# Performance work log

Hardware: AMD Instinct MI355X
Metric: run time of the kernel (lower is better)

## Reference

```python
import jax, jax.numpy as jnp
import numpy as np


def _dwconv_silu(feat, w, b):
    # feat: (B, L, C); depthwise 1D conv, kernel 7, pad 3, then SiLU (PointLiteConv)
    x = jnp.swapaxes(feat, 1, 2)  # (B, C, L)
    y = jax.lax.conv_general_dilated(x, w, (1,), [(3, 3)],
                                     feature_group_count=x.shape[1],
                                     dimension_numbers=('NCH', 'OIH', 'NCH'))
    y = y + b[None, :, None]
    return jnp.swapaxes(jax.nn.silu(y), 1, 2)


def _issm_scan(x, h0, dt, A, Bm, Cm, Dp):
    # x: (B,L,H,P)  h0: (B,H,P,N)  dt: (B,L,H,N)  A: (H,1)  Bm,Cm: (B,L,1,N)  Dp: (H,)
    dA = jnp.exp(dt * A)                      # (B,L,H,N) discrete decay
    u = dt * Bm                               # (B,L,H,N) input coeff (ngroups=1 broadcast)
    Cb = jnp.broadcast_to(Cm, dt.shape)       # (B,L,H,N)

    def step(h, inp):
        dA_t, u_t, x_t, c_t = inp             # (B,H,N),(B,H,N),(B,H,P),(B,H,N)
        h = dA_t[:, :, None, :] * h + x_t[..., None] * u_t[:, :, None, :]
        return h, jnp.einsum('bhpn,bhn->bhp', h, c_t)

    xs = tuple(jnp.moveaxis(a, 1, 0) for a in (dA, u, x, Cb))
    hF, ys = jax.lax.scan(step, h0, xs)
    y = jnp.moveaxis(ys, 0, 1) + Dp[None, None, :, None] * x
    return y, hF


def setup_inputs() -> dict:
    key = jax.random.key(0)
    ks = jax.random.split(key, 20)
    B, L, K = 2, 2048, 64
    d_model, d_state, d_dist, H, G, d_inner = 512, 64, 4, 8, 1, 1024
    c_conv = d_inner + 2 * G  # 1026
    s = 0.02
    dt0 = jnp.exp(jax.random.uniform(ks[12], (H,)) * (np.log(0.1) - np.log(1e-4)) + np.log(1e-4))
    dt0 = jnp.clip(dt0, 1e-4, None)
    return {
        'in_key': jax.random.normal(ks[0], (B, L, d_model), jnp.float32),
        'in_query': jax.random.normal(ks[1], (B, K, d_model), jnp.float32),
        'dist': jax.random.uniform(ks[2], (B, L, K, d_dist), jnp.float32),
        'key_xyz': jax.random.normal(ks[3], (B, L, 3), jnp.float32),
        'key_proj_w': jax.random.normal(ks[4], (2 * d_inner + 2 * G + H, d_model), jnp.float32) * s,
        'key_conv_w': jax.random.normal(ks[5], (c_conv, 1, 7), jnp.float32) * s,
        'key_conv_b': jnp.zeros((c_conv,), jnp.float32),
        'key_conv_back_w': jax.random.normal(ks[6], (c_conv, 1, 7), jnp.float32) * s,
        'key_conv_back_b': jnp.zeros((c_conv,), jnp.float32),
        'query_proj_w': jax.random.normal(ks[7], (d_inner, d_model), jnp.float32) * s,
        'bc_proj_w': jax.random.normal(ks[8], (2 * G, d_dist), jnp.float32) * s,
        'dt_proj_w': jax.random.normal(ks[9], (H, d_dist), jnp.float32) * s,
        'dt_bias': dt0 + jnp.log(-jnp.expm1(-dt0)),
        'A_log': jnp.log(jax.random.uniform(ks[10], (H,), jnp.float32, 1.0, 16.0)),
        'D_param': jnp.ones((H,), jnp.float32),
        'out_key_w': jax.random.normal(ks[11], (d_model, d_inner), jnp.float32) * s,
        'out_query_w': jax.random.normal(ks[13], (d_model, d_inner), jnp.float32) * s,
        'key_norm_w': jnp.ones((d_inner,), jnp.float32),
        'q_ln_w': jnp.ones((d_inner,), jnp.float32),
        'q_ln_b': jnp.zeros((d_inner,), jnp.float32),
    }


def reference(in_key, in_query, dist, key_xyz, key_proj_w, key_conv_w, key_conv_b,
              key_conv_back_w, key_conv_back_b, query_proj_w, bc_proj_w, dt_proj_w,
              dt_bias, A_log, D_param, out_key_w, out_query_w, key_norm_w, q_ln_w, q_ln_b):
    B, L, _ = in_key.shape
    K = in_query.shape[1]
    d_inner = query_proj_w.shape[0]
    H = dt_bias.shape[0]
    G = bc_proj_w.shape[0] // 2
    P = d_inner // H

    zxbcdt = in_key @ key_proj_w.T                       # (B,L,2*di+2G+H)
    z = zxbcdt[..., :d_inner]
    xbc = zxbcdt[..., d_inner:2 * d_inner + 2 * G]
    dt_head = zxbcdt[..., 2 * d_inner + 2 * G:]          # (B,L,H)

    xbc_f = _dwconv_silu(xbc, key_conv_w, key_conv_b)
    x = xbc_f[..., :d_inner]
    b_bias = xbc_f[..., d_inner:d_inner + G]
    c_bias = xbc_f[..., d_inner + G:]
    xbc_b = _dwconv_silu(xbc, key_conv_back_w, key_conv_back_b)
    x_bk = xbc_b[..., :d_inner]
    b_bias_b = xbc_b[..., d_inner:d_inner + G]
    c_bias_b = xbc_b[..., d_inner + G:]

    # initial state: 'b l (h hd) -> b h hd l'  -> (B,H,P,K)
    h0 = (in_query @ query_proj_w.T).reshape(B, K, H, P).transpose(0, 2, 3, 1)
    A = -jnp.exp(A_log)[:, None]                         # (H,1), repeated over d_state

    bc = dist @ bc_proj_w.T                              # (B,L,K,2G)
    b_base = jnp.swapaxes(bc[..., :G], -1, -2)           # (B,L,G,K)
    c_base = jnp.swapaxes(bc[..., G:], -1, -2)
    Bm = b_base + b_bias[..., None]
    Cm = c_base + c_bias[..., None]
    Bmb = b_base + b_bias_b[..., None]
    Cmb = c_base + c_bias_b[..., None]

    dt = jax.nn.softplus(jnp.swapaxes(dist @ dt_proj_w.T, -1, -2)
                         + dt_head[..., None] + dt_bias[None, None, :, None])  # (B,L,H,K)

    xh = x.reshape(B, L, H, P)
    y_f, h_f = _issm_scan(xh, h0, dt, A, Bm, Cm, D_param)
    xb = jnp.flip(x_bk.reshape(B, L, H, P), 1)
    y_b, h_b = _issm_scan(xb, h0, jnp.flip(dt, 1), A, jnp.flip(Bmb, 1), jnp.flip(Cmb, 1), D_param)
    y = (y_f + jnp.flip(y_b, 1)) * 0.5                   # (B,L,H,P)
    h_last = (h_f + h_b) * 0.5                           # (B,H,P,K)

    key_feat = y.reshape(B, L, d_inner)
    xg = key_feat * jax.nn.silu(z)                       # gated RMSNorm (gate before norm)
    key_n = xg * jax.lax.rsqrt(jnp.mean(xg * xg, -1, keepdims=True) + 1e-5) * key_norm_w
    out_key = key_n @ out_key_w.T

    q = h_last.transpose(0, 3, 1, 2).reshape(B, K, d_inner)  # 'b h p l -> b l (h p)'
    mu = jnp.mean(q, -1, keepdims=True)
    var = jnp.mean((q - mu) ** 2, -1, keepdims=True)
    qn = (q - mu) * jax.lax.rsqrt(var + 1e-5) * q_ln_w + q_ln_b
    out_query = qn @ out_query_w.T
    return out_key, out_query
```

## Files before the change

kernel.cpp:

```cpp
#include <hip/hip_runtime.h>
#include <hip/hip_bf16.h>
#include <cstdint>

constexpr int B_ = 2, L_ = 2048, K_ = 64, H_ = 8, P_ = 128, DI = 1024;
constexpr int NPROJ = 2058;
constexpr int NC = L_ / 64;
constexpr int XBCS = 1040;

typedef unsigned short u16;
typedef short bf16x8 __attribute__((ext_vector_type(8)));
typedef float f32x4 __attribute__((ext_vector_type(4)));

__constant__ int c_sz[20] = {2097152,65536,1048576,12288,1053696,7182,1026,7182,1026,
                             524288,8,32,8,8,8,524288,524288,1024,1024,1024};
__constant__ int c_of[20] = {16,2097168,2162704,3211280,3223568,4277264,4284446,4285472,
                             4292654,4293680,4817968,4817976,4818008,4818016,4818024,
                             4818032,5342320,5866608,5867632,5868656};
constexpr int OF_INKEY = 16, OF_INQ = 2097168, OF_DIST = 2162704, OF_KPW = 3223568;
constexpr int OF_CONVW = 4277264, OF_CONVB = 4284446, OF_CONVBW = 4285472, OF_CONVBB = 4292654;
constexpr int OF_QPW = 4293680, OF_BCW = 4817968, OF_DTW = 4817976, OF_DTBIAS = 4818008;
constexpr int OF_ALOG = 4818016, OF_D = 4818024, OF_OKW = 4818032, OF_OQW = 5342320;
constexpr int OF_KNW = 5866608, OF_QLW = 5867632, OF_QLB = 5868656;
constexpr int SEG_A = 2097152, SEG_W = 2176*512, SEG_O = 524288;
constexpr int SEG_Q = 65536, SEG_P = 524288, SEG_D = 1048576;
constexpr int NSMALL = 18552;
constexpr int NSTAGE = SEG_O + SEG_O + 4096 + NSMALL + (SEG_A + SEG_Q + SEG_D + SEG_W + SEG_P);

constexpr int WZ     = 5869696;
constexpr int WXBC   = 10064000;
constexpr int WDTH   = 14266496;
constexpr int WXF    = 14299264;
constexpr int WXBK   = 18493568;
constexpr int WBBF   = 22687872;
constexpr int WCBF   = 22691968;
constexpr int WBBB   = 22696064;
constexpr int WCBB   = 22700160;
constexpr int WDT    = 22704256;
constexpr int WBBASE = 24801408;
constexpr int WCBASE = 25063552;
constexpr int WH0I   = 25325696;
constexpr int WE     = 25456768;
constexpr int WDH    = 25522304;
constexpr int WYF    = 42299520;
constexpr int WYB    = 46493824;
constexpr int WHFIN  = 50688128;
constexpr int WSROW  = 50950272;
constexpr int WEND   = 50954368;

#define DEV __device__ __forceinline__
DEV float4 ld4(const float* p) { return *(const float4*)p; }
DEV void st4(float* p, float4 v) { *(float4*)p = v; }
DEV float silu_(float x) { return x / (1.f + __expf(-x)); }
DEV u16 f2b(float f) {
    unsigned x = __float_as_uint(f);
    return (u16)((x + 0x7fffu + ((x >> 16) & 1u)) >> 16);
}
DEV float b2f(u16 v) { return __uint_as_float(((unsigned)v) << 16); }
DEV float4 b2f4(const u16* p) {
    uint2 u = *(const uint2*)p;
    float4 r;
    r.x = __uint_as_float(u.x << 16);
    r.y = __uint_as_float(u.x & 0xffff0000u);
    r.z = __uint_as_float(u.y << 16);
    r.w = __uint_as_float(u.y & 0xffff0000u);
    return r;
}
DEV float4 b2f4u(uint2 u) {
    float4 r;
    r.x = __uint_as_float(u.x << 16);
    r.y = __uint_as_float(u.x & 0xffff0000u);
    r.z = __uint_as_float(u.y << 16);
    r.w = __uint_as_float(u.y & 0xffff0000u);
    return r;
}
DEV uint2 pku2(float4 v) {
    uint2 u;
    u.x = (unsigned)f2b(v.x) | ((unsigned)f2b(v.y) << 16);
    u.y = (unsigned)f2b(v.z) | ((unsigned)f2b(v.w) << 16);
    return u;
}
DEV void st4b(u16* p, float4 v) { *(uint2*)p = pku2(v); }

#define GLL16(gp, lp) __builtin_amdgcn_global_load_lds( \
    (const __attribute__((address_space(1))) unsigned int*)(gp), \
    (__attribute__((address_space(3))) unsigned int*)(lp), 16, 0, 0)

struct SrcPtrs { const void* p[20]; };
DEV bool bfmode(const SrcPtrs& sp) { return ((const u16*)sp.p[17])[0] == 0x3F80u; }

__global__ void k_sentinel(float* out) { out[threadIdx.x] = 1e9f; }

__global__ __launch_bounds__(256) void k_stage(SrcPtrs sp, float* ws) {
    int g = blockIdx.x * 256 + threadIdx.x;
    bool bf = bfmode(sp);
    if (g < SEG_O) {
        int col = g & 1023;
        float wv = bf ? b2f(((const u16*)sp.p[15])[g]) : ((const float*)sp.p[15])[g];
        float kn = bf ? b2f(((const u16*)sp.p[17])[col]) : ((const float*)sp.p[17])[col];
        ((u16*)(ws + OF_OKW))[g] = f2b(wv * kn);
        return;
    }
    g -= SEG_O;
    if (g < SEG_O) {
        ((u16*)(ws + OF_OQW))[g] = bf ? ((const u16*)sp.p[16])[g]
                                      : f2b(((const float*)sp.p[16])[g]);
        return;
    }
    g -= SEG_O;
    if (g < 4096) { ws[WSROW + g] = 0.f; return; }
    g -= 4096;
    if (g < NSMALL) {
        const int sidx[12] = {5,6,7,8,10,11,12,13,14,17,18,19};
        int rem = g;
        #pragma unroll
        for (int ii = 0; ii < 12; ++ii) {
            int s = sidx[ii];
            int sz = c_sz[s];
            if (rem < sz) {
                float v = bf ? b2f(((const u16*)sp.p[s])[rem])
                             : ((const float*)sp.p[s])[rem];
                ws[c_of[s] + rem] = v;
                return;
            }
            rem -= sz;
        }
        return;
    }
    g -= NSMALL;
    if (bf) return;
    if (g < SEG_A) { ((u16*)(ws + OF_INKEY))[g] = f2b(((const float*)sp.p[0])[g]); return; }
    g -= SEG_A;
    if (g < SEG_Q) { ((u16*)(ws + OF_INQ))[g] = f2b(((const float*)sp.p[1])[g]); return; }
    g -= SEG_Q;
    if (g < SEG_D) { ws[OF_DIST + g] = ((const float*)sp.p[2])[g]; return; }
    g -= SEG_D;
    if (g < SEG_W) {
        int row = g >> 9, col = g & 511;
        ((u16*)(ws + OF_KPW))[g] = (row < NPROJ) ? f2b(((const float*)sp.p[4])[row*512 + col]) : (u16)0;
        return;
    }
    g -= SEG_W;
    if (g < SEG_P) { ((u16*)(ws + OF_QPW))[g] = f2b(((const float*)sp.p[9])[g]); return; }
}

__global__ __launch_bounds__(256) void k_gemm_proj(SrcPtrs sp, float* ws) {
    __shared__ u16 As[128*32], Bs[128*32];
    bool bf = bfmode(sp);
    int tid = threadIdx.x, w = tid >> 6, l = tid & 63;
    int wm = w & 1, wn = w >> 1;
    int lr = l & 15, lq = l >> 4;
    int srow = tid >> 2, scol = (tid & 3) * 8;
    if (blockIdx.y == 32) {
        if (blockIdx.x >= 8) return;
        const u16* Ab = bf ? (const u16*)sp.p[1] : (const u16*)(ws + OF_INQ);
        const u16* Wb = bf ? (const u16*)sp.p[9] : (const u16*)(ws + OF_QPW);
        int n0 = blockIdx.x * 128;
        f32x4 acc[4][4];
        #pragma unroll
        for (int i = 0; i < 4; ++i)
            #pragma unroll
            for (int j = 0; j < 4; ++j) acc[i][j] = {0.f,0.f,0.f,0.f};
        for (int kt = 0; kt < 512; kt += 32) {
            __syncthreads();
            GLL16(Ab + (size_t)(srow)*512      + kt + scol, As + (w*512));
            GLL16(Ab + (size_t)(64 + srow)*512 + kt + scol, As + (2048 + w*512));
            GLL16(Wb + (size_t)(n0 + srow)*512      + kt + scol, Bs + (w*512));
            GLL16(Wb + (size_t)(n0 + 64 + srow)*512 + kt + scol, Bs + (2048 + w*512));
            __syncthreads();
            bf16x8 af[4], bfr[4];
            #pragma unroll
            for (int mi = 0; mi < 4; ++mi) af[mi]  = *(const bf16x8*)&As[(wm*64 + mi*16 + lr)*32 + lq*8];
            #pragma unroll
            for (int ni = 0; ni < 4; ++ni) bfr[ni] = *(const bf16x8*)&Bs[(wn*64 + ni*16 + lr)*32 + lq*8];
            #pragma unroll
            for (int mi = 0; mi < 4; ++mi)
                #pragma unroll
                for (int ni = 0; ni < 4; ++ni)
                    acc[mi][ni] = __builtin_amdgcn_mfma_f32_16x16x32_bf16(af[mi], bfr[ni], acc[mi][ni], 0, 0, 0);
        }
        #pragma unroll
        for (int mi = 0; mi < 4; ++mi)
            #pragma unroll
            for (int ni = 0; ni < 4; ++ni)
                #pragma unroll
                for (int r = 0; r < 4; ++r) {
                    int m = wm*64 + mi*16 + lq*4 + r;
                    int n = n0 + wn*64 + ni*16 + lr;
                    int b = m >> 6, kq = m & 63, h = n >> 7, p = n & 127;
                    ws[WH0I + ((b*8 + h)*64 + kq)*128 + p] = acc[mi][ni][r];
                }
        return;
    }
    const u16* Ab = bf ? (const u16*)sp.p[0] : (const u16*)(ws + OF_INKEY);
    const u16* Wb = bf ? (const u16*)sp.p[4] : (const u16*)(ws + OF_KPW);
    int n0 = blockIdx.x * 128, m0 = blockIdx.y * 128;
    int wr0 = n0 + srow;      if (wr0 > NPROJ-1) wr0 = NPROJ-1;
    int wr1 = n0 + 64 + srow; if (wr1 > NPROJ-1) wr1 = NPROJ-1;
    f32x4 acc[4][4];
    #pragma unroll
    for (int i = 0; i < 4; ++i)
        #pragma unroll
        for (int j = 0; j < 4; ++j) acc[i][j] = {0.f,0.f,0.f,0.f};
    for (int kt = 0; kt < 512; kt += 32) {
        __syncthreads();
        GLL16(Ab + (size_t)(m0 + srow)*512      + kt + scol, As + (w*512));
        GLL16(Ab + (size_t)(m0 + 64 + srow)*512 + kt + scol, As + (2048 + w*512));
        GLL16(Wb + (size_t)wr0*512 + kt + scol, Bs + (w*512));
        GLL16(Wb + (size_t)wr1*512 + kt + scol, Bs + (2048 + w*512));
        __syncthreads();
        bf16x8 af[4], bfr[4];
        #pragma unroll
        for (int mi = 0; mi < 4; ++mi) af[mi]  = *(const bf16x8*)&As[(wm*64 + mi*16 + lr)*32 + lq*8];
        #pragma unroll
        for (int ni = 0; ni < 4; ++ni) bfr[ni] = *(const bf16x8*)&Bs[(wn*64 + ni*16 + lr)*32 + lq*8];
        #pragma unroll
        for (int mi = 0; mi < 4; ++mi)
            #pragma unroll
            for (int ni = 0; ni < 4; ++ni)
                acc[mi][ni] = __builtin_amdgcn_mfma_f32_16x16x32_bf16(af[mi], bfr[ni], acc[mi][ni], 0, 0, 0);
    }
    u16* xbc = (u16*)(ws + WXBC);
    u16* zb  = (u16*)(ws + WZ);
    #pragma unroll
    for (int mi = 0; mi < 4; ++mi)
        #pragma unroll
        for (int ni = 0; ni < 4; ++ni)
            #pragma unroll
            for (int r = 0; r < 4; ++r) {
                int m = m0 + wm*64 + mi*16 + lq*4 + r;
                int n = n0 + wn*64 + ni*16 + lr;
                if (n >= NPROJ) continue;
                float v = acc[mi][ni][r];
                if (n < 1024)       zb[m*1024 + n] = f2b(v);
                else if (n < 2050)  xbc[m*XBCS + (n-1024)] = f2b(v);
                else                ws[WDTH + m*8 + (n-2050)] = v;
            }
}

__global__ __launch_bounds__(256) void k_mid(SrcPtrs sp, float* ws) {
    int bx = blockIdx.x, tid = threadIdx.x;
    if (bx < 1280) {
        int cb = bx >> 8, tile = bx & 255;
        int bl0 = tile * 16;
        int l0 = bl0 & (L_ - 1);
        int base = bl0 - l0;
        int cch = cb * 256 + tid;
        if (cb == 4) { if (tid >= 2) return; cch = 1024 + tid; }
        const u16* xbc = (const u16*)(ws + WXBC);
        const float* wfp = ws + OF_CONVW + cch*7;
        const float* wbp = ws + OF_CONVBW + cch*7;
        float wf[7], wb[7];
        #pragma unroll
        for (int j = 0; j < 7; ++j) { wf[j] = wfp[j]; wb[j] = wbp[j]; }
        float bfv = ws[OF_CONVB + cch], bbv = ws[OF_CONVBB + cch];
        float win[22];
        #pragma unroll
        for (int j = 0; j < 22; ++j) {
            int l2 = l0 - 3 + j;
            win[j] = (l2 >= 0 && l2 < L_) ? b2f(xbc[(base + l2)*XBCS + cch]) : 0.f;
        }
        u16* XF = (u16*)(ws + WXF);
        u16* XB = (u16*)(ws + WXBK);
        #pragma unroll
        for (int i = 0; i < 16; ++i) {
            float af = bfv, ab = bbv;
            #pragma unroll
            for (int j = 0; j < 7; ++j) { af += win[i+j]*wf[j]; ab += win[i+j]*wb[j]; }
            af = silu_(af); ab = silu_(ab);
            if (cb < 4) {
                XF[(bl0 + i)*1024 + cch] = f2b(af);
                XB[(bl0 + i)*1024 + cch] = f2b(ab);
            } else if (cch == 1024) {
                ws[WBBF + bl0 + i] = af; ws[WBBB + bl0 + i] = ab;
            } else {
                ws[WCBF + bl0 + i] = af; ws[WCBB + bl0 + i] = ab;
            }
        }
        return;
    }
    {
        bool bf = bfmode(sp);
        int g = (bx - 1280) * 256 + tid;
        int k = g & 63, bl = g >> 6;
        float4 d4;
        if (bf) d4 = b2f4((const u16*)sp.p[2] + (size_t)g*4);
        else    d4 = ld4(&ws[OF_DIST + g*4]);
        const float* bcw = ws + OF_BCW;
        ws[WBBASE + g] = d4.x*bcw[0] + d4.y*bcw[1] + d4.z*bcw[2] + d4.w*bcw[3];
        ws[WCBASE + g] = d4.x*bcw[4] + d4.y*bcw[5] + d4.z*bcw[6] + d4.w*bcw[7];
        const float* dtw = ws + OF_DTW;
        const float* dtb = ws + OF_DTBIAS;
        const float* dth = ws + WDTH + bl*8;
        #pragma unroll
        for (int h = 0; h < 8; ++h) {
            float t = d4.x*dtw[h*4] + d4.y*dtw[h*4+1] + d4.z*dtw[h*4+2] + d4.w*dtw[h*4+3]
                    + dth[h] + dtb[h];
            float sp2 = (t > 20.f) ? t : log1pf(__expf(t));
            ws[WDT + (bl*8 + h)*64 + k] = sp2;
        }
    }
}

__global__ __launch_bounds__(256, 3) void k_scanA(float* ws) {
    __shared__ float scs[4096];
    __shared__ u16 sUeD[64*72];
    __shared__ u16 sCe[64*72];
    __shared__ u16 sM[64*72];
    __shared__ u16 sUeO[32*72];
    __shared__ float sG[128];
    u16* sXt = (u16*)scs;
    int bx = blockIdx.x;
    int c = bx & 31, dir = (bx >> 5) & 1, h = (bx >> 6) & 7, b = bx >> 9;
    int tid = threadIdx.x, w = tid >> 6, l = tid & 63;
    int lr = l & 15, tq = l >> 4;
    float Ah = -__expf(ws[OF_ALOG + h]);
    float Dv = ws[OF_D + h];
    const float* dt = ws + WDT;
    const float* bbase = ws + WBBASE; const float* cbase = ws + WCBASE;
    const float* bbias = ws + (dir ? WBBB : WBBF);
    const float* cbias = ws + (dir ? WCBB : WCBF);
    for (int q = tid; q < 1024; q += 256) {
        int t = q >> 4, k4 = (q & 15) << 2;
        int gt = dir ? (L_ - 1 - (c*64 + t)) : (c*64 + t);
        int bl = b*L_ + gt;
        float4 dv = ld4(&dt[(bl*8 + h)*64 + k4]);
        float4 bb4 = ld4(&bbase[bl*64 + k4]);
        float4 cb4 = ld4(&cbase[bl*64 + k4]);
        float bbv = bbias[bl], cbv = cbias[bl];
        st4(&scs[t*64 + k4], make_float4(dv.x*Ah, dv.y*Ah, dv.z*Ah, dv.w*Ah));
        st4b(&sUeD[t*72 + k4], make_float4(dv.x*(bb4.x+bbv), dv.y*(bb4.y+bbv),
                                           dv.z*(bb4.z+bbv), dv.w*(bb4.w+bbv)));
        st4b(&sCe[t*72 + k4], make_float4(cb4.x+cbv, cb4.y+cbv, cb4.z+cbv, cb4.w+cbv));
    }
    __syncthreads();
    {
        float* tmp = (float*)sUeO;
        int kk = tid & 63, seg = tid >> 6;
        float run = 0.f;
        for (int t = seg*16; t < seg*16 + 16; ++t) { run += scs[t*64 + kk]; scs[t*64 + kk] = run; }
        tmp[seg*64 + kk] = run;
        __syncthreads();
        float off = 0.f;
        for (int s2 = 0; s2 < seg; ++s2) off += tmp[s2*64 + kk];
        if (seg == 3) ws[WE + (((b*8 + h)*2 + dir)*32 + c)*64 + kk] = __expf(off + run);
        __syncthreads();
        if (seg > 0)
            for (int t = seg*16; t < seg*16 + 16; ++t) scs[t*64 + kk] += off;
    }
    __syncthreads();
    for (int q = tid; q < 2048; q += 256) {
        int s = q >> 6, k = q & 63;
        sUeO[s*72 + k] = f2b(b2f(sUeD[s*72 + k]) * __expf(scs[2048 + k] - scs[s*64 + k]));
    }
    if (tid < 128) {
        int j = tid >> 6, k = tid & 63;
        sG[tid] = __expf(scs[63*64 + k] - scs[j*2048 + k]);
    }
    {
        uint4 z4 = make_uint4(0,0,0,0);
        for (int q = tid; q < 576; q += 256) ((uint4*)sM)[q] = z4;
    }
    __syncthreads();
    for (int q = tid; q < 4096; q += 256) {
        int t = q >> 6, k = q & 63;
        int t0 = (t >> 5) << 5;
        sCe[t*72 + k] = f2b(b2f(sCe[t*72 + k]) * __expf(scs[t*64 + k] - scs[t0*64 + k]));
    }
    for (int q = tid; q < 4096; q += 256) {
        int s = q >> 6, k = q & 63;
        int t0 = (s >> 5) << 5;
        sUeD[s*72 + k] = f2b(b2f(sUeD[s*72 + k]) * __expf(scs[t0*64 + k] - scs[s*64 + k]));
    }
    __syncthreads();
    {
        constexpr unsigned TTP = 1047188u;
        constexpr unsigned SSP = 936208u;
        for (int i = w; i < 10; i += 4) {
            int ttile = (TTP >> (2*i)) & 3, stile = (SSP >> (2*i)) & 3;
            const u16* Bb = (ttile >= 2 && stile < 2) ? sUeO : sUeD;
            f32x4 acc = {0.f, 0.f, 0.f, 0.f};
            #pragma unroll
            for (int kh = 0; kh < 2; ++kh) {
                bf16x8 a  = *(const bf16x8*)&sCe[(ttile*16 + lr)*72 + kh*32 + tq*8];
                bf16x8 bb = *(const bf16x8*)&Bb [(stile*16 + lr)*72 + kh*32 + tq*8];
                acc = __builtin_amdgcn_mfma_f32_16x16x32_bf16(a, bb, acc, 0, 0, 0);
            }
            #pragma unroll
            for (int r = 0; r < 4; ++r) {
                int row = ttile*16 + tq*4 + r, col = stile*16 + lr;
                sM[row*72 + col] = f2b(row >= col ? acc[r] : 0.f);
            }
        }
    }
    __syncthreads();
    for (int q = tid; q < 4096; q += 256) {
        int k = q >> 6, s = q & 63;
        sCe[k*72 + s] = f2b(b2f(sUeD[s*72 + k]) * sG[((s >> 5) << 6) + k]);
    }
    __syncthreads();
    bf16x8 aM[2], aU[2];
    #pragma unroll
    for (int kh = 0; kh < 2; ++kh) {
        aM[kh] = *(const bf16x8*)&sM [(w*16 + lr)*72 + kh*32 + tq*8];
        aU[kh] = *(const bf16x8*)&sCe[(w*16 + lr)*72 + kh*32 + tq*8];
    }
    __syncthreads();
    u16* sYst = sM;
    u16* sDst = sCe;
    u16* yloc16 = (u16*)(ws + (dir ? WYB : WYF));
    const u16* Xsrc = (const u16*)(ws + (dir ? WXBK : WXF));
    u16* DH = (u16*)(ws + WDH);
    int bhd = (b*8 + h)*2 + dir;
    for (int ph = 0; ph < 2; ++ph) {
        #pragma unroll
        for (int g3 = 0; g3 < 2; ++g3) {
            int t0 = w*16 + g3*8;
            u16 x[8];
            #pragma unroll
            for (int j = 0; j < 8; ++j) {
                int row = c*64 + t0 + j;
                int gt = dir ? (L_ - 1 - row) : row;
                x[j] = Xsrc[(b*L_ + gt)*1024 + h*128 + ph*64 + l];
            }
            uint4 qv;
            qv.x = (unsigned)x[0] | ((unsigned)x[1] << 16);
            qv.y = (unsigned)x[2] | ((unsigned)x[3] << 16);
            qv.z = (unsigned)x[4] | ((unsigned)x[5] << 16);
            qv.w = (unsigned)x[6] | ((unsigned)x[7] << 16);
            *(uint4*)&sXt[l*72 + t0] = qv;
        }
        __syncthreads();
        f32x4 accY[4], accD[4];
        #pragma unroll
        for (int pi = 0; pi < 4; ++pi) { accY[pi] = {0.f,0.f,0.f,0.f}; accD[pi] = {0.f,0.f,0.f,0.f}; }
        #pragma unroll
        for (int pi = 0; pi < 4; ++pi) {
            bf16x8 bX0 = *(const bf16x8*)&sXt[(pi*16 + lr)*72 +  0 + tq*8];
            bf16x8 bX1 = *(const bf16x8*)&sXt[(pi*16 + lr)*72 + 32 + tq*8];
            accY[pi] = __builtin_amdgcn_mfma_f32_16x16x32_bf16(aM[0], bX0, accY[pi], 0, 0, 0);
            accY[pi] = __builtin_amdgcn_mfma_f32_16x16x32_bf16(aM[1], bX1, accY[pi], 0, 0, 0);
            accD[pi] = __builtin_amdgcn_mfma_f32_16x16x32_bf16(aU[0], bX0, accD[pi], 0, 0, 0);
            accD[pi] = __builtin_amdgcn_mfma_f32_16x16x32_bf16(aU[1], bX1, accD[pi], 0, 0, 0);
        }
        #pragma unroll
        for (int pi = 0; pi < 4; ++pi) {
            int p = pi*16 + lr;
            #pragma unroll
            for (int r = 0; r < 4; ++r) {
                int t = w*16 + tq*4 + r;
                float xv = b2f(sXt[p*72 + t]);
                sYst[t*64 + (((pi + t) & 3) << 4) + lr] = f2b(accY[pi][r] + Dv*xv);
                sDst[t*64 + (((pi + t) & 3) << 4) + lr] = f2b(accD[pi][r]);
            }
        }
        __syncthreads();
        {
            int t2 = tid >> 2, cg = tid & 3;
            int swz = ((cg + t2) & 3) << 4;
            int gt2 = dir ? (L_ - 1 - (c*64 + t2)) : (c*64 + t2);
            uint4 y0 = *(uint4*)&sYst[t2*64 + swz];
            uint4 d0 = *(uint4*)&sDst[t2*64 + swz];
            u16* yp = yloc16 + (size_t)(b*L_ + gt2)*1024 + h*128 + ph*64 + cg*16;
            u16* dp = DH + (size_t)((bhd*32 + c)*64 + t2)*128 + ph*64 + cg*16;
            *(uint4*)yp = y0;
            *(uint4*)dp = d0;
            uint4 y1 = *(uint4*)&sYst[t2*64 + swz + 8];
            uint4 d1 = *(uint4*)&sDst[t2*64 + swz + 8];
            *(uint4*)(yp + 8) = y1;
            *(uint4*)(dp + 8) = d1;
        }
        __syncthreads();
    }
}

__global__ __launch_bounds__(256) void k_carry(float* ws) {
    int bx = blockIdx.x;
    int pg = bx & 7, dir = (bx >> 3) & 1, h = (bx >> 4) & 7, b = bx >> 7;
    int tid = threadIdx.x;
    int k = tid >> 2, p = pg*16 + (tid & 3)*4;
    int bhd = (b*8 + h)*2 + dir;
    float ear[NC];
    const float* Eb = ws + WE + bhd*32*64 + k;
    #pragma unroll
    for (int c = 0; c < NC; ++c) ear[c] = Eb[c*64];
    float4 hr = ld4(&ws[WH0I + ((b*8 + h)*64 + k)*128 + p]);
    u16* DH = (u16*)(ws + WDH);
    size_t base0 = (size_t)(bhd*32*64 + k)*128 + p;
    uint2 dbuf[4];
    #pragma unroll
    for (int i = 0; i < 4; ++i) dbuf[i] = *(const uint2*)&DH[base0 + (size_t)i*8192];
    #pragma unroll
    for (int c = 0; c < NC; ++c) {
        float4 d = b2f4u(dbuf[c & 3]);
        *(uint2*)&DH[base0 + (size_t)c*8192] = pku2(hr);
        if (c + 4 < NC) dbuf[c & 3] = *(const uint2*)&DH[base0 + (size_t)(c + 4)*8192];
        float e = ear[c];
        hr.x = e*hr.x + d.x; hr.y = e*hr.y + d.y; hr.z = e*hr.z + d.z; hr.w = e*hr.w + d.w;
    }
    st4(&ws[WHFIN + (bhd*64 + k)*128 + p], hr);
}

__global__ __launch_bounds__(256, 3) void k_scanB(float* ws) {
    __shared__ float scs[4096];
    __shared__ u16 sCf[64*72], sCb[64*72];
    __shared__ u16 sHf[64*72], sHb[64*72];
    int bx = blockIdx.x;
    int tid = threadIdx.x;
    if (bx >= 512) {
        int bk = bx - 512;
        int b = bk >> 6, kq = bk & 63;
        float* sq = scs;
        float* red1 = (float*)sCf;
        float* red2 = red1 + 4;
        float* sstat = red2 + 4;
        for (int i = tid; i < 1024; i += 256) {
            int h = i >> 7, p = i & 127;
            int i0 = (((b*8 + h)*2 + 0)*64 + kq)*128 + p;
            int i1 = (((b*8 + h)*2 + 1)*64 + kq)*128 + p;
            sq[i] = 0.5f * (ws[WHFIN + i0] + ws[WHFIN + i1]);
        }
        __syncthreads();
        float4 v = ld4(&sq[tid*4]);
        float s1 = v.x + v.y + v.z + v.w;
        float s2 = v.x*v.x + v.y*v.y + v.z*v.z + v.w*v.w;
        #pragma unroll
        for (int o = 32; o > 0; o >>= 1) { s1 += __shfl_down(s1, o); s2 += __shfl_down(s2, o); }
        if ((tid & 63) == 0) { red1[tid >> 6] = s1; red2[tid >> 6] = s2; }
        __syncthreads();
        if (tid == 0) {
            float S1 = red1[0]+red1[1]+red1[2]+red1[3];
            float S2 = red2[0]+red2[1]+red2[2]+red2[3];
            float mu = S1 * (1.f/1024.f);
            float var = S2 * (1.f/1024.f) - mu*mu;
            sstat[0] = mu; sstat[1] = rsqrtf(var + 1e-5f);
        }
        __syncthreads();
        float mu = sstat[0], rs = sstat[1];
        u16* qn = (u16*)(ws + WXBC);
        float4 kw = ld4(&ws[OF_QLW + tid*4]);
        float4 kb = ld4(&ws[OF_QLB + tid*4]);
        st4b(qn + bk*1024 + tid*4,
             make_float4((v.x - mu)*rs*kw.x + kb.x, (v.y - mu)*rs*kw.y + kb.y,
                         (v.z - mu)*rs*kw.z + kb.z, (v.w - mu)*rs*kw.w + kb.w));
        return;
    }
    int j = bx & 31, h = (bx >> 5) & 7, b = bx >> 8;
    int w = tid >> 6, l = tid & 63;
    int lr = l & 15, tq = l >> 4;
    float Ah = -__expf(ws[OF_ALOG + h]);
    for (int q = tid; q < 1024; q += 256) {
        int t = q >> 4, k4 = (q & 15) << 2;
        int bl = b*L_ + j*64 + t;
        float4 dv = ld4(&ws[WDT + (bl*8 + h)*64 + k4]);
        st4(&scs[t*64 + k4], make_float4(dv.x*Ah, dv.y*Ah, dv.z*Ah, dv.w*Ah));
    }
    __syncthreads();
    {
        float* tmp = (float*)sCf;
        int kk = tid & 63, seg = tid >> 6;
        float run = 0.f;
        for (int t = seg*16; t < seg*16 + 16; ++t) { run += scs[t*64 + kk]; scs[t*64 + kk] = run; }
        tmp[seg*64 + kk] = run;
        __syncthreads();
        float off = 0.f;
        for (int s2 = 0; s2 < seg; ++s2) off += tmp[s2*64 + kk];
        __syncthreads();
        if (seg > 0)
            for (int t = seg*16; t < seg*16 + 16; ++t) scs[t*64 + kk] += off;
    }
    __syncthreads();
    for (int q = tid; q < 4096; q += 256) {
        int t = q >> 6, k = q & 63;
        int bl = b*L_ + j*64 + t;
        float pref = scs[t*64 + k];
        float prev = (t == 0) ? 0.f : scs[(t-1)*64 + k];
        float tot  = scs[63*64 + k];
        float cb0 = ws[WCBASE + bl*64 + k];
        sCf[t*72 + k] = f2b((cb0 + ws[WCBF + bl]) * __expf(pref));
        sCb[t*72 + k] = f2b((cb0 + ws[WCBB + bl]) * __expf(tot - prev));
    }
    const u16* h0f = (const u16*)(ws + WDH) + (size_t)((((b*8 + h)*2 + 0)*32 + j)*64)*128;
    const u16* h0b = (const u16*)(ws + WDH) + (size_t)((((b*8 + h)*2 + 1)*32 + (31 - j))*64)*128;
    __syncthreads();
    bf16x8 af[2], ab_[2];
    #pragma unroll
    for (int kh = 0; kh < 2; ++kh) {
        af[kh]  = *(const bf16x8*)&sCf[(w*16 + lr)*72 + kh*32 + tq*8];
        ab_[kh] = *(const bf16x8*)&sCb[(w*16 + lr)*72 + kh*32 + tq*8];
    }
    const u16* yf16 = (const u16*)(ws + WYF);
    const u16* yb16 = (const u16*)(ws + WYB);
    const u16* zb   = (const u16*)(ws + WZ);
    u16* xgb = (u16*)(ws + WXF);
    u16* sYf = sCf;
    u16* sYb = sCb;
    u16* sZ  = sHf;
    u16* sO  = sHb;
    float ssr[4] = {0.f, 0.f, 0.f, 0.f};
    for (int ph = 0; ph < 2; ++ph) {
        #pragma unroll
        for (int g2 = 0; g2 < 2; ++g2) {
            int k0 = w*16 + g2*8;
            u16 xf[8], xb[8];
            #pragma unroll
            for (int jj = 0; jj < 8; ++jj) {
                xf[jj] = h0f[(k0 + jj)*128 + ph*64 + l];
                xb[jj] = h0b[(k0 + jj)*128 + ph*64 + l];
            }
            uint4 qf, qb;
            qf.x = (unsigned)xf[0] | ((unsigned)xf[1] << 16);
            qf.y = (unsigned)xf[2] | ((unsigned)xf[3] << 16);
            qf.z = (unsigned)xf[4] | ((unsigned)xf[5] << 16);
            qf.w = (unsigned)xf[6] | ((unsigned)xf[7] << 16);
            qb.x = (unsigned)xb[0] | ((unsigned)xb[1] << 16);
            qb.y = (unsigned)xb[2] | ((unsigned)xb[3] << 16);
            qb.z = (unsigned)xb[4] | ((unsigned)xb[5] << 16);
            qb.w = (unsigned)xb[6] | ((unsigned)xb[7] << 16);
            *(uint4*)&sHf[l*72 + k0] = qf;
            *(uint4*)&sHb[l*72 + k0] = qb;
        }
        __syncthreads();
        f32x4 accf[4], accb[4];
        #pragma unroll
        for (int pi = 0; pi < 4; ++pi) { accf[pi] = {0.f,0.f,0.f,0.f}; accb[pi] = {0.f,0.f,0.f,0.f}; }
        #pragma unroll
        for (int pi = 0; pi < 4; ++pi) {
            bf16x8 bf0 = *(const bf16x8*)&sHf[(pi*16 + lr)*72 +  0 + tq*8];
            bf16x8 bf1 = *(const bf16x8*)&sHf[(pi*16 + lr)*72 + 32 + tq*8];
            bf16x8 bb0 = *(const bf16x8*)&sHb[(pi*16 + lr)*72 +  0 + tq*8];
            bf16x8 bb1 = *(const bf16x8*)&sHb[(pi*16 + lr)*72 + 32 + tq*8];
            accf[pi] = __builtin_amdgcn_mfma_f32_16x16x32_bf16(af[0],  bf0, accf[pi], 0, 0, 0);
            accf[pi] = __builtin_amdgcn_mfma_f32_16x16x32_bf16(af[1],  bf1, accf[pi], 0, 0, 0);
            accb[pi] = __builtin_amdgcn_mfma_f32_16x16x32_bf16(ab_[0], bb0, accb[pi], 0, 0, 0);
            accb[pi] = __builtin_amdgcn_mfma_f32_16x16x32_bf16(ab_[1], bb1, accb[pi], 0, 0, 0);
        }
        __syncthreads();
        {
            int t2 = tid >> 2, cg = tid & 3;
            int swz = ((cg + t2) & 3) << 4;
            size_t off = (size_t)(b*L_ + j*64 + t2)*1024 + h*128 + ph*64 + cg*16;
            uint4 a0 = *(const uint4*)(yf16 + off);
            uint4 a1 = *(const uint4*)(yf16 + off + 8);
            uint4 b0 = *(const uint4*)(yb16 + off);
            uint4 b1 = *(const uint4*)(yb16 + off + 8);
            uint4 c0 = *(const uint4*)(zb + off);
            uint4 c1 = *(const uint4*)(zb + off + 8);
            *(uint4*)&sYf[t2*64 + swz] = a0; *(uint4*)&sYf[t2*64 + swz + 8] = a1;
            *(uint4*)&sYb[t2*64 + swz] = b0; *(uint4*)&sYb[t2*64 + swz + 8] = b1;
            *(uint4*)&sZ [t2*64 + swz] = c0; *(uint4*)&sZ [t2*64 + swz + 8] = c1;
        }
        __syncthreads();
        #pragma unroll
        for (int pi = 0; pi < 4; ++pi) {
            #pragma unroll
            for (int r = 0; r < 4; ++r) {
                int t = w*16 + tq*4 + r;
                int sidx = t*64 + (((pi + t) & 3) << 4) + lr;
                float yf = b2f(sYf[sidx]), yb = b2f(sYb[sidx]), zv = b2f(sZ[sidx]);
                float o = 0.5f*(yf + yb + accf[pi][r] + accb[pi][r]) * silu_(zv);
                ssr[r] += o*o;
                sO[sidx] = f2b(o);
            }
        }
        __syncthreads();
        {
            int t2 = tid >> 2, cg = tid & 3;
            int swz = ((cg + t2) & 3) << 4;
            uint4 o0 = *(uint4*)&sO[t2*64 + swz];
            uint4 o1 = *(uint4*)&sO[t2*64 + swz + 8];
            u16* op = xgb + (size_t)(b*L_ + j*64 + t2)*1024 + h*128 + ph*64 + cg*16;
            *(uint4*)op = o0;
            *(uint4*)(op + 8) = o1;
        }
        __syncthreads();
    }
    #pragma unroll
    for (int r = 0; r < 4; ++r) {
        float v = ssr[r];
        v += __shfl_xor(v, 1); v += __shfl_xor(v, 2);
        v += __shfl_xor(v, 4); v += __shfl_xor(v, 8);
        if (lr == 0)
            atomicAdd(&ws[WSROW + b*L_ + j*64 + w*16 + tq*4 + r], v);
    }
}

__global__ __launch_bounds__(256) void k_outkey(float* ws, void* d_out, const void* in17) {
    __shared__ u16 As[128*32], Bs[128*32];
    int tid = threadIdx.x, w = tid >> 6, l = tid & 63;
    int wm = w & 1, wn = w >> 1;
    int lr = l & 15, lq = l >> 4;
    int srow = tid >> 2, scol = (tid & 3) * 8;
    bool bf = (((const u16*)in17)[0] == 0x3F80u);
    if (blockIdx.y == 32) {
        if (blockIdx.x >= 4) return;
        const u16* Ab = (const u16*)(ws + WXBC);
        const u16* Wb = (const u16*)(ws + OF_OQW);
        int n0 = blockIdx.x * 128;
        f32x4 acc[4][4];
        #pragma unroll
        for (int i = 0; i < 4; ++i)
            #pragma unroll
            for (int jj = 0; jj < 4; ++jj) acc[i][jj] = {0.f,0.f,0.f,0.f};
        for (int kt = 0; kt < 1024; kt += 32) {
            __syncthreads();
            GLL16(Ab + (size_t)(srow)*1024      + kt + scol, As + (w*512));
            GLL16(Ab + (size_t)(64 + srow)*1024 + kt + scol, As + (2048 + w*512));
            GLL16(Wb + (size_t)(n0 + srow)*1024      + kt + scol, Bs + (w*512));
            GLL16(Wb + (size_t)(n0 + 64 + srow)*1024 + kt + scol, Bs + (2048 + w*512));
            __syncthreads();
            bf16x8 af[4], bfr[4];
            #pragma unroll
            for (int mi = 0; mi < 4; ++mi) af[mi]  = *(const bf16x8*)&As[(wm*64 + mi*16 + lr)*32 + lq*8];
            #pragma unroll
            for (int ni = 0; ni < 4; ++ni) bfr[ni] = *(const bf16x8*)&Bs[(wn*64 + ni*16 + lr)*32 + lq*8];
            #pragma unroll
            for (int mi = 0; mi < 4; ++mi)
                #pragma unroll
                for (int ni = 0; ni < 4; ++ni)
                    acc[mi][ni] = __builtin_amdgcn_mfma_f32_16x16x32_bf16(af[mi], bfr[ni], acc[mi][ni], 0, 0, 0);
        }
        #pragma unroll
        for (int mi = 0; mi < 4; ++mi)
            #pragma unroll
            for (int ni = 0; ni < 4; ++ni)
                #pragma unroll
                for (int r = 0; r < 4; ++r) {
                    int m = wm*64 + mi*16 + lq*4 + r;
                    int n = n0 + wn*64 + ni*16 + lr;
                    if (n >= 512) continue;
                    int idx = 2097152 + m*512 + n;
                    float v = acc[mi][ni][r];
                    if (bf) ((__hip_bfloat16*)d_out)[idx] = __float2bfloat16(v);
                    else    ((float*)d_out)[idx] = v;
                }
        return;
    }
    const u16* Ab = (const u16*)(ws + WXF);
    const u16* Wb = (const u16*)(ws + OF_OKW);
    int n0 = blockIdx.x * 64, m0 = blockIdx.y * 128;
    f32x4 acc[4][2];
    #pragma unroll
    for (int i = 0; i < 4; ++i) { acc[i][0] = {0.f,0.f,0.f,0.f}; acc[i][1] = {0.f,0.f,0.f,0.f}; }
    for (int kt = 0; kt < 1024; kt += 32) {
        __syncthreads();
        GLL16(Ab + (size_t)(m0 + srow)*1024      + kt + scol, As + (w*512));
        GLL16(Ab + (size_t)(m0 + 64 + srow)*1024 + kt + scol, As + (2048 + w*512));
        GLL16(Wb + (size_t)(n0 + srow)*1024      + kt + scol, Bs + (w*512));
        __syncthreads();
        bf16x8 af[4], bfr[2];
        #pragma unroll
        for (int mi = 0; mi < 4; ++mi) af[mi]  = *(const bf16x8*)&As[(wm*64 + mi*16 + lr)*32 + lq*8];
        #pragma unroll
        for (int ni = 0; ni < 2; ++ni) bfr[ni] = *(const bf16x8*)&Bs[(wn*32 + ni*16 + lr)*32 + lq*8];
        #pragma unroll
        for (int mi = 0; mi < 4; ++mi)
            #pragma unroll
            for (int ni = 0; ni < 2; ++ni)
                acc[mi][ni] = __builtin_amdgcn_mfma_f32_16x16x32_bf16(af[mi], bfr[ni], acc[mi][ni], 0, 0, 0);
    }
    #pragma unroll
    for (int mi = 0; mi < 4; ++mi)
        #pragma unroll
        for (int r = 0; r < 4; ++r) {
            int m = m0 + wm*64 + mi*16 + lq*4 + r;
            float rs = rsqrtf(ws[WSROW + m] * (1.f/1024.f) + 1e-5f);
            #pragma unroll
            for (int ni = 0; ni < 2; ++ni) {
                int n = n0 + wn*32 + ni*16 + lr;
                int idx = m*512 + n;
                float v = acc[mi][ni][r] * rs;
                if (bf) ((__hip_bfloat16*)d_out)[idx] = __float2bfloat16(v);
                else    ((float*)d_out)[idx] = v;
            }
        }
}

extern "C" void kernel_launch(void* const* d_in, const int* in_sizes, int n_in,
                              void* d_out, int out_size, void* d_ws, size_t ws_size,
                              hipStream_t stream) {
    float* ws = (float*)d_ws;
    if (ws_size < (size_t)WEND * sizeof(float)) {
        k_sentinel<<<1, 64, 0, stream>>>((float*)d_out);
        return;
    }
    SrcPtrs sp;
    for (int i = 0; i < 20; ++i) sp.p[i] = d_in[i];
    k_stage<<<(NSTAGE + 255)/256, 256, 0, stream>>>(sp, ws);
    k_gemm_proj<<<dim3(17, 33), 256, 0, stream>>>(sp, ws);
    k_mid<<<2304, 256, 0, stream>>>(sp, ws);
    k_scanA<<<1024, 256, 0, stream>>>(ws);
    k_carry<<<256, 256, 0, stream>>>(ws);
    k_scanB<<<640, 256, 0, stream>>>(ws);
    k_outkey<<<dim3(8, 33), 256, 0, stream>>>(ws, d_out, d_in[17]);
}
```

Before: 273.0 us.

## Shrink staging grid, fuse scanA exp passes, preload all carry chunks

```diff
diff --git a/kernel.cpp b/kernel.cpp
--- a/kernel.cpp
+++ b/kernel.cpp
@@ -24,7 +24,8 @@
 constexpr int SEG_A = 2097152, SEG_W = 2176*512, SEG_O = 524288;
 constexpr int SEG_Q = 65536, SEG_P = 524288, SEG_D = 1048576;
 constexpr int NSMALL = 18552;
-constexpr int NSTAGE = SEG_O + SEG_O + 4096 + NSMALL + (SEG_A + SEG_Q + SEG_D + SEG_W + SEG_P);
+constexpr int NBF16W = SEG_O + SEG_O + 4096 + NSMALL;
+constexpr long FPTOT = (long)SEG_A + SEG_Q + SEG_D + SEG_W + SEG_P;
 
 constexpr int WZ     = 5869696;
 constexpr int WXBC   = 10064000;
@@ -93,54 +94,59 @@
 __global__ __launch_bounds__(256) void k_stage(SrcPtrs sp, float* ws) {
     int g = blockIdx.x * 256 + threadIdx.x;
     bool bf = bfmode(sp);
-    if (g < SEG_O) {
-        int col = g & 1023;
-        float wv = bf ? b2f(((const u16*)sp.p[15])[g]) : ((const float*)sp.p[15])[g];
-        float kn = bf ? b2f(((const u16*)sp.p[17])[col]) : ((const float*)sp.p[17])[col];
-        ((u16*)(ws + OF_OKW))[g] = f2b(wv * kn);
-        return;
-    }
-    g -= SEG_O;
-    if (g < SEG_O) {
-        ((u16*)(ws + OF_OQW))[g] = bf ? ((const u16*)sp.p[16])[g]
-                                      : f2b(((const float*)sp.p[16])[g]);
-        return;
-    }
-    g -= SEG_O;
-    if (g < 4096) { ws[WSROW + g] = 0.f; return; }
-    g -= 4096;
-    if (g < NSMALL) {
-        const int sidx[12] = {5,6,7,8,10,11,12,13,14,17,18,19};
-        int rem = g;
-        #pragma unroll
-        for (int ii = 0; ii < 12; ++ii) {
-            int s = sidx[ii];
-            int sz = c_sz[s];
-            if (rem < sz) {
-                float v = bf ? b2f(((const u16*)sp.p[s])[rem])
-                             : ((const float*)sp.p[s])[rem];
-                ws[c_of[s] + rem] = v;
-                return;
+    if (g < NBF16W) {
+        int r = g;
+        if (r < SEG_O) {
+            int col = r & 1023;
+            float wv = bf ? b2f(((const u16*)sp.p[15])[r]) : ((const float*)sp.p[15])[r];
+            float kn = bf ? b2f(((const u16*)sp.p[17])[col]) : ((const float*)sp.p[17])[col];
+            ((u16*)(ws + OF_OKW))[r] = f2b(wv * kn);
+            goto tail;
+        }
+        r -= SEG_O;
+        if (r < SEG_O) {
+            ((u16*)(ws + OF_OQW))[r] = bf ? ((const u16*)sp.p[16])[r]
+                                          : f2b(((const float*)sp.p[16])[r]);
+            goto tail;
+        }
+        r -= SEG_O;
+        if (r < 4096) { ws[WSROW + r] = 0.f; goto tail; }
+        r -= 4096;
+        {
+            const int sidx[12] = {5,6,7,8,10,11,12,13,14,17,18,19};
+            #pragma unroll
+            for (int ii = 0; ii < 12; ++ii) {
+                int s = sidx[ii];
+                int sz = c_sz[s];
+                if (r < sz) {
+                    float v = bf ? b2f(((const u16*)sp.p[s])[r])
+                                 : ((const float*)sp.p[s])[r];
+                    ws[c_of[s] + r] = v;
+                    break;
+                }
+                r -= sz;
             }
-            rem -= sz;
-        }
-        return;
-    }
-    g -= NSMALL;
+        }
+    }
+tail:
     if (bf) return;
-    if (g < SEG_A) { ((u16*)(ws + OF_INKEY))[g] = f2b(((const float*)sp.p[0])[g]); return; }
-    g -= SEG_A;
-    if (g < SEG_Q) { ((u16*)(ws + OF_INQ))[g] = f2b(((const float*)sp.p[1])[g]); return; }
-    g -= SEG_Q;
-    if (g < SEG_D) { ws[OF_DIST + g] = ((const float*)sp.p[2])[g]; return; }
-    g -= SEG_D;
-    if (g < SEG_W) {
-        int row = g >> 9, col = g & 511;
-        ((u16*)(ws + OF_KPW))[g] = (row < NPROJ) ? f2b(((const float*)sp.p[4])[row*512 + col]) : (u16)0;
-        return;
-    }
-    g -= SEG_W;
-    if (g < SEG_P) { ((u16*)(ws + OF_QPW))[g] = f2b(((const float*)sp.p[9])[g]); return; }
+    long stride = (long)gridDim.x * 256;
+    for (long q = g; q < FPTOT; q += stride) {
+        long r = q;
+        if (r < SEG_A) { ((u16*)(ws + OF_INKEY))[r] = f2b(((const float*)sp.p[0])[r]); continue; }
+        r -= SEG_A;
+        if (r < SEG_Q) { ((u16*)(ws + OF_INQ))[r] = f2b(((const float*)sp.p[1])[r]); continue; }
+        r -= SEG_Q;
+        if (r < SEG_D) { ws[OF_DIST + r] = ((const float*)sp.p[2])[r]; continue; }
+        r -= SEG_D;
+        if (r < SEG_W) {
+            int row = (int)(r >> 9), col = (int)(r & 511);
+            ((u16*)(ws + OF_KPW))[r] = (row < NPROJ) ? f2b(((const float*)sp.p[4])[row*512 + col]) : (u16)0;
+            continue;
+        }
+        r -= SEG_W;
+        ((u16*)(ws + OF_QPW))[r] = f2b(((const float*)sp.p[9])[r]);
+    }
 }
 
 __global__ __launch_bounds__(256) void k_gemm_proj(SrcPtrs sp, float* ws) {
@@ -307,7 +313,7 @@
     __shared__ u16 sCe[64*72];
     __shared__ u16 sM[64*72];
     __shared__ u16 sUeO[32*72];
-    __shared__ float sG[128];
+    __shared__ float sG[192];
     u16* sXt = (u16*)scs;
     int bx = blockIdx.x;
     int c = bx & 31, dir = (bx >> 5) & 1, h = (bx >> 6) & 7, b = bx >> 9;
@@ -348,47 +354,56 @@
             for (int t = seg*16; t < seg*16 + 16; ++t) scs[t*64 + kk] += off;
     }
     __syncthreads();
-    for (int q = tid; q < 2048; q += 256) {
-        int s = q >> 6, k = q & 63;
-        sUeO[s*72 + k] = f2b(b2f(sUeD[s*72 + k]) * __expf(scs[2048 + k] - scs[s*64 + k]));
-    }
-    if (tid < 128) {
+    if (tid < 192) {
         int j = tid >> 6, k = tid & 63;
-        sG[tid] = __expf(scs[63*64 + k] - scs[j*2048 + k]);
-    }
-    {
-        uint4 z4 = make_uint4(0,0,0,0);
-        for (int q = tid; q < 576; q += 256) ((uint4*)sM)[q] = z4;
+        float v;
+        if (j < 2) v = __expf(scs[63*64 + k] - scs[j*2048 + k]);
+        else       v = __expf(scs[2048 + k] - scs[k]);
+        sG[tid] = v;
     }
     __syncthreads();
     for (int q = tid; q < 4096; q += 256) {
         int t = q >> 6, k = q & 63;
         int t0 = (t >> 5) << 5;
-        sCe[t*72 + k] = f2b(b2f(sCe[t*72 + k]) * __expf(scs[t*64 + k] - scs[t0*64 + k]));
-    }
-    for (int q = tid; q < 4096; q += 256) {
+        float d = scs[t*64 + k] - scs[t0*64 + k];
+        float e1 = __expf(d);
+        float e2 = __expf(-d);
+        sCe [t*72 + k] = f2b(b2f(sCe [t*72 + k]) * e1);
+        sUeD[t*72 + k] = f2b(b2f(sUeD[t*72 + k]) * e2);
+    }
+    __syncthreads();
+    for (int q = tid; q < 2048; q += 256) {
         int s = q >> 6, k = q & 63;
-        int t0 = (s >> 5) << 5;
-        sUeD[s*72 + k] = f2b(b2f(sUeD[s*72 + k]) * __expf(scs[t0*64 + k] - scs[s*64 + k]));
+        sUeO[s*72 + k] = f2b(b2f(sUeD[s*72 + k]) * sG[128 + k]);
     }
     __syncthreads();
     {
         constexpr unsigned TTP = 1047188u;
         constexpr unsigned SSP = 936208u;
-        for (int i = w; i < 10; i += 4) {
-            int ttile = (TTP >> (2*i)) & 3, stile = (SSP >> (2*i)) & 3;
-            const u16* Bb = (ttile >= 2 && stile < 2) ? sUeO : sUeD;
-            f32x4 acc = {0.f, 0.f, 0.f, 0.f};
-            #pragma unroll
-            for (int kh = 0; kh < 2; ++kh) {
-                bf16x8 a  = *(const bf16x8*)&sCe[(ttile*16 + lr)*72 + kh*32 + tq*8];
-                bf16x8 bb = *(const bf16x8*)&Bb [(stile*16 + lr)*72 + kh*32 + tq*8];
-                acc = __builtin_amdgcn_mfma_f32_16x16x32_bf16(a, bb, acc, 0, 0, 0);
-            }
-            #pragma unroll
-            for (int r = 0; r < 4; ++r) {
-                int row = ttile*16 + tq*4 + r, col = stile*16 + lr;
-                sM[row*72 + col] = f2b(row >= col ? acc[r] : 0.f);
+        constexpr unsigned UTT = 2368u;
+        constexpr unsigned USS = 4025u;
+        for (int i = w; i < 16; i += 4) {
+            if (i < 10) {
+                int ttile = (TTP >> (2*i)) & 3, stile = (SSP >> (2*i)) & 3;
+                const u16* Bb = (ttile >= 2 && stile < 2) ? sUeO : sUeD;
+                f32x4 acc = {0.f, 0.f, 0.f, 0.f};
+                #pragma unroll
+                for (int kh = 0; kh < 2; ++kh) {
+                    bf16x8 a  = *(const bf16x8*)&sCe[(ttile*16 + lr)*72 + kh*32 + tq*8];
+                    bf16x8 bb = *(const bf16x8*)&Bb [(stile*16 + lr)*72 + kh*32 + tq*8];
+                    acc = __builtin_amdgcn_mfma_f32_16x16x32_bf16(a, bb, acc, 0, 0, 0);
+                }
+                #pragma unroll
+                for (int r = 0; r < 4; ++r) {
+                    int row = ttile*16 + tq*4 + r, col = stile*16 + lr;
+                    sM[row*72 + col] = f2b(row >= col ? acc[r] : 0.f);
+                }
+            } else {
+                int j2 = i - 10;
+                int ttile = (UTT >> (2*j2)) & 3, stile = (USS >> (2*j2)) & 3;
+                #pragma unroll
+                for (int r = 0; r < 4; ++r)
+                    sM[(ttile*16 + tq*4 + r)*72 + stile*16 + lr] = 0;
             }
         }
     }
@@ -486,14 +501,13 @@
     float4 hr = ld4(&ws[WH0I + ((b*8 + h)*64 + k)*128 + p]);
     u16* DH = (u16*)(ws + WDH);
     size_t base0 = (size_t)(bhd*32*64 + k)*128 + p;
-    uint2 dbuf[4];
-    #pragma unroll
-    for (int i = 0; i < 4; ++i) dbuf[i] = *(const uint2*)&DH[base0 + (size_t)i*8192];
+    uint2 dbuf[NC];
+    #pragma unroll
+    for (int c = 0; c < NC; ++c) dbuf[c] = *(const uint2*)&DH[base0 + (size_t)c*8192];
     #pragma unroll
     for (int c = 0; c < NC; ++c) {
-        float4 d = b2f4u(dbuf[c & 3]);
+        float4 d = b2f4u(dbuf[c]);
         *(uint2*)&DH[base0 + (size_t)c*8192] = pku2(hr);
-        if (c + 4 < NC) dbuf[c & 3] = *(const uint2*)&DH[base0 + (size_t)(c + 4)*8192];
         float e = ear[c];
         hr.x = e*hr.x + d.x; hr.y = e*hr.y + d.y; hr.z = e*hr.z + d.z; hr.w = e*hr.w + d.w;
     }
@@ -785,7 +799,7 @@
     }
     SrcPtrs sp;
     for (int i = 0; i < 20; ++i) sp.p[i] = d_in[i];
-    k_stage<<<(NSTAGE + 255)/256, 256, 0, stream>>>(sp, ws);
+    k_stage<<<(NBF16W + 255)/256, 256, 0, stream>>>(sp, ws);
     k_gemm_proj<<<dim3(17, 33), 256, 0, stream>>>(sp, ws);
     k_mid<<<2304, 256, 0, stream>>>(sp, ws);
     k_scanA<<<1024, 256, 0, stream>>>(ws);
```

Result: no change. 269.5 us (-1.3%).
